# Optimization experiments

Measured on AMD Instinct MI355X. Metric: run time of the kernel, lower is better.

Reference implementation:

```python
import jax, jax.numpy as jnp
import numpy as np

POOL = (7, 7)


def crop_and_resize(image, boxes, box_idx, crop_size):
    """Faithful jnp port of tf.image.crop_and_resize (bilinear, extrapolation_value=0).

    image: [B, H, W, C]; boxes: [N, 4] normalized (y1, x1, y2, x2); box_idx: [N] int.
    Returns [N, ph, pw, C].
    """
    H, W = image.shape[1], image.shape[2]
    ph, pw = crop_size
    y1, x1, y2, x2 = boxes[:, 0], boxes[:, 1], boxes[:, 2], boxes[:, 3]
    iy = jnp.arange(ph, dtype=image.dtype)
    ix = jnp.arange(pw, dtype=image.dtype)
    # sample coords in source-pixel space, TF convention for crop_size > 1
    ys = y1[:, None] * (H - 1) + iy[None, :] * ((y2 - y1)[:, None] * (H - 1) / (ph - 1))  # [N, ph]
    xs = x1[:, None] * (W - 1) + ix[None, :] * ((x2 - x1)[:, None] * (W - 1) / (pw - 1))  # [N, pw]
    vy = (ys >= 0) & (ys <= H - 1)
    vx = (xs >= 0) & (xs <= W - 1)
    y0 = jnp.floor(ys)
    x0 = jnp.floor(xs)
    wy = (ys - y0)[:, :, None, None]   # [N, ph, 1, 1]
    wx = (xs - x0)[:, None, :, None]   # [N, 1, pw, 1]
    y0i = jnp.clip(y0, 0, H - 1).astype(jnp.int32)
    y1i = jnp.clip(y0 + 1, 0, H - 1).astype(jnp.int32)  # when ys is integral, wy==0 so clamp is harmless
    x0i = jnp.clip(x0, 0, W - 1).astype(jnp.int32)
    x1i = jnp.clip(x0 + 1, 0, W - 1).astype(jnp.int32)
    b = box_idx[:, None, None]

    def g(yi, xi):
        return image[b, yi[:, :, None], xi[:, None, :], :]  # [N, ph, pw, C]

    top = g(y0i, x0i) * (1 - wx) + g(y0i, x1i) * wx
    bot = g(y1i, x0i) * (1 - wx) + g(y1i, x1i) * wx
    out = top * (1 - wy) + bot * wy
    valid = (vy[:, :, None] & vx[:, None, :])[..., None]
    return jnp.where(valid, out, jnp.zeros((), image.dtype))


def setup_inputs() -> dict:
    key = jax.random.key(0)
    kb, kp, k3, k4, k5 = jax.random.split(key, 5)
    B, N, C = 2, 1000, 256
    # valid normalized boxes: per-axis sorted uniforms -> y1 <= y2, x1 <= x2
    raw = jax.random.uniform(kb, (B, N, 2, 2), dtype=jnp.float32)  # [..., (y|x), (lo,hi)]
    raw = jnp.sort(raw, axis=-1)
    boxes = jnp.stack([raw[..., 0, 0], raw[..., 1, 0], raw[..., 0, 1], raw[..., 1, 1]], axis=-1)
    return {
        "boxes": boxes,
        "positive_indices": jax.random.randint(kp, (B, N), 0, 2, dtype=jnp.int32),
        "p3": jax.random.normal(k3, (B, 128, 128, C), dtype=jnp.float32),
        "p4": jax.random.normal(k4, (B, 64, 64, C), dtype=jnp.float32),
        "p5": jax.random.normal(k5, (B, 32, 32, C), dtype=jnp.float32),
        "config": 0,
    }


def reference(boxes, positive_indices, p3, p4, p5, config):
    B, N = boxes.shape[0], boxes.shape[1]
    ph, pw = POOL
    h = boxes[..., 2] - boxes[..., 0]
    w = boxes[..., 3] - boxes[..., 1]
    # roi_level = clip(ceil(5 + log2(h*w)), 3, 5); clip in float first (log2(0) -> -inf)
    lvl = jnp.ceil(5.0 + jnp.log(h * w) / jnp.log(2.0))
    roi_level = jnp.clip(lvl, 3.0, 5.0).astype(jnp.int32)  # [B, N]
    boxes_flat = jax.lax.stop_gradient(boxes.reshape(B * N, 4))  # boxes get no grad in original
    lvl_flat = roi_level.reshape(B * N)
    box_idx = jnp.repeat(jnp.arange(B, dtype=jnp.int32), N)
    C = p3.shape[-1]
    pooled = jnp.zeros((B * N, ph, pw, C), dtype=p3.dtype)
    for level, feat in zip((3, 4, 5), (p3, p4, p5)):
        crop = crop_and_resize(feat, boxes_flat, box_idx, POOL)
        mask = (lvl_flat == level)[:, None, None, None]
        pooled = jnp.where(mask, crop, pooled)
    return pooled.reshape(B, N, ph, pw, C)
```

## Files before the change

kernel.cpp:

```cpp
#include <hip/hip_runtime.h>
#include <math.h>


#define N_PER_B 1000
#define NBOX    2000
#define CCH     256
#define PH      7
#define PW      7

__global__ __launch_bounds__(448, 4) void pyramid_roi_align_kernel(
    const float* __restrict__ boxes,
    const float* __restrict__ p3,
    const float* __restrict__ p4,
    const float* __restrict__ p5,
    float* __restrict__ out)
{
    const int box  = blockIdx.x;
    const int iy   = threadIdx.x >> 6;
    const int lane = threadIdx.x & 63;
    const int c    = lane * 4;

    const float y1 = boxes[box * 4 + 0];
    const float x1 = boxes[box * 4 + 1];
    const float y2 = boxes[box * 4 + 2];
    const float x2 = boxes[box * 4 + 3];
    const float h  = y2 - y1;
    const float w  = x2 - x1;

    const float lvl  = ceilf(5.0f + logf(h * w) / 0.69314718055994530942f);
    const float lvlc = fminf(fmaxf(lvl, 3.0f), 5.0f);
    const int level  = (int)lvlc;

    const float* feat;
    int H;
    if (level <= 3)      { feat = p3; H = 128; }
    else if (level == 4) { feat = p4; H = 64;  }
    else                 { feat = p5; H = 32;  }
    const int W = H;

    const int b = (box >= N_PER_B) ? 1 : 0;
    feat += (size_t)b * H * W * CCH;

    const float Hm1 = (float)(H - 1);
    const float Wm1 = (float)(W - 1);

    const float ys = y1 * Hm1 + (float)iy * (h * Hm1 / 6.0f);
    const bool  vy = (ys >= 0.0f) && (ys <= Hm1);

    const float y0f = floorf(ys);
    const float wy  = ys - y0f;
    const float omwy = 1.0f - wy;

    const int y0i = (int)fminf(fmaxf(y0f,        0.0f), Hm1);
    const int y1i = (int)fminf(fmaxf(y0f + 1.0f, 0.0f), Hm1);

    const float* row0 = feat + (size_t)y0i * W * CCH + c;
    const float* row1 = feat + (size_t)y1i * W * CCH + c;

    const float xstep = w * Wm1 / 6.0f;
    float* dst_base = out + ((size_t)box * (PH * PW) + (size_t)iy * PW) * CCH + c;

#pragma unroll
    for (int ix = 0; ix < PW; ++ix) {
        const float xs = x1 * Wm1 + (float)ix * xstep;
        const bool  vx = (xs >= 0.0f) && (xs <= Wm1);

        const float x0f = floorf(xs);
        const float wx  = xs - x0f;
        const float omwx = 1.0f - wx;

        const int x0i = (int)fminf(fmaxf(x0f,        0.0f), Wm1);
        const int x1i = (int)fminf(fmaxf(x0f + 1.0f, 0.0f), Wm1);

        const float4 v00 = *(const float4*)(row0 + (size_t)x0i * CCH);
        const float4 v01 = *(const float4*)(row0 + (size_t)x1i * CCH);
        const float4 v10 = *(const float4*)(row1 + (size_t)x0i * CCH);
        const float4 v11 = *(const float4*)(row1 + (size_t)x1i * CCH);

        float4 res;
        res.x = (v00.x * omwx + v01.x * wx) * omwy + (v10.x * omwx + v11.x * wx) * wy;
        res.y = (v00.y * omwx + v01.y * wx) * omwy + (v10.y * omwx + v11.y * wx) * wy;
        res.z = (v00.z * omwx + v01.z * wx) * omwy + (v10.z * omwx + v11.z * wx) * wy;
        res.w = (v00.w * omwx + v01.w * wx) * omwy + (v10.w * omwx + v11.w * wx) * wy;

        if (!(vy && vx)) { res.x = 0.0f; res.y = 0.0f; res.z = 0.0f; res.w = 0.0f; }

        *(float4*)(dst_base + (size_t)ix * CCH) = res;
    }
}

extern "C" void kernel_launch(void* const* d_in, const int* in_sizes, int n_in,
                              void* d_out, int out_size, void* d_ws, size_t ws_size,
                              hipStream_t stream) {
    const float* boxes = (const float*)d_in[0];
    const float* p3 = (const float*)d_in[2];
    const float* p4 = (const float*)d_in[3];
    const float* p5 = (const float*)d_in[4];
    float* out = (float*)d_out;

    hipLaunchKernelGGL(pyramid_roi_align_kernel, dim3(NBOX), dim3(448), 0, stream,
                       boxes, p3, p4, p5, out);
}
```

Before: 168.9 us.

## Batch all gathers before compute, nontemporal stores, remap waves to 256-thread blocks

Each wave now handles one (box, row) pair and blocks carry 4 waves instead of 7, which changes the block/grid decomposition. All 28 float4 gathers for a row are issued up front, before any interpolation, to raise memory-level parallelism. Output stores become nontemporal so the large write stream does not evict cached feature data. The batched loads raise register pressure, which may lower occupancy.

```diff
diff --git a/kernel.cpp b/kernel.cpp
--- a/kernel.cpp
+++ b/kernel.cpp
@@ -7,18 +7,24 @@
 #define CCH     256
 #define PH      7
 #define PW      7
+#define WAVES_PER_BLOCK 4
+#define TOTAL_WAVES (NBOX * PH)
 
-__global__ __launch_bounds__(448, 4) void pyramid_roi_align_kernel(
+typedef float nfloat4 __attribute__((ext_vector_type(4)));
+
+__global__ __launch_bounds__(256, 3) void pyramid_roi_align_kernel(
     const float* __restrict__ boxes,
     const float* __restrict__ p3,
     const float* __restrict__ p4,
     const float* __restrict__ p5,
     float* __restrict__ out)
 {
-    const int box  = blockIdx.x;
-    const int iy   = threadIdx.x >> 6;
+    const int wave = blockIdx.x * WAVES_PER_BLOCK + (threadIdx.x >> 6);
     const int lane = threadIdx.x & 63;
     const int c    = lane * 4;
+
+    const int box = wave / PH;
+    const int iy  = wave - box * PH;
 
     const float y1 = boxes[box * 4 + 0];
     const float x1 = boxes[box * 4 + 1];
@@ -47,8 +53,8 @@
     const float ys = y1 * Hm1 + (float)iy * (h * Hm1 / 6.0f);
     const bool  vy = (ys >= 0.0f) && (ys <= Hm1);
 
-    const float y0f = floorf(ys);
-    const float wy  = ys - y0f;
+    const float y0f  = floorf(ys);
+    const float wy   = ys - y0f;
     const float omwy = 1.0f - wy;
 
     const int y0i = (int)fminf(fmaxf(y0f,        0.0f), Hm1);
@@ -58,34 +64,38 @@
     const float* row1 = feat + (size_t)y1i * W * CCH + c;
 
     const float xstep = w * Wm1 / 6.0f;
+
+    nfloat4 v00[PW], v01[PW], v10[PW], v11[PW];
+    float   wxv[PW];
+    bool    vxv[PW];
+
+#pragma unroll
+    for (int ix = 0; ix < PW; ++ix) {
+        const float xs = x1 * Wm1 + (float)ix * xstep;
+        vxv[ix] = (xs >= 0.0f) && (xs <= Wm1);
+        const float x0f = floorf(xs);
+        wxv[ix] = xs - x0f;
+        const int x0i = (int)fminf(fmaxf(x0f,        0.0f), Wm1);
+        const int x1i = (int)fminf(fmaxf(x0f + 1.0f, 0.0f), Wm1);
+        v00[ix] = *(const nfloat4*)(row0 + (size_t)x0i * CCH);
+        v01[ix] = *(const nfloat4*)(row0 + (size_t)x1i * CCH);
+        v10[ix] = *(const nfloat4*)(row1 + (size_t)x0i * CCH);
+        v11[ix] = *(const nfloat4*)(row1 + (size_t)x1i * CCH);
+    }
+
     float* dst_base = out + ((size_t)box * (PH * PW) + (size_t)iy * PW) * CCH + c;
 
 #pragma unroll
     for (int ix = 0; ix < PW; ++ix) {
-        const float xs = x1 * Wm1 + (float)ix * xstep;
-        const bool  vx = (xs >= 0.0f) && (xs <= Wm1);
-
-        const float x0f = floorf(xs);
-        const float wx  = xs - x0f;
+        const float wx   = wxv[ix];
         const float omwx = 1.0f - wx;
 
-        const int x0i = (int)fminf(fmaxf(x0f,        0.0f), Wm1);
-        const int x1i = (int)fminf(fmaxf(x0f + 1.0f, 0.0f), Wm1);
+        nfloat4 res = (v00[ix] * omwx + v01[ix] * wx) * omwy
+                    + (v10[ix] * omwx + v11[ix] * wx) * wy;
 
-        const float4 v00 = *(const float4*)(row0 + (size_t)x0i * CCH);
-        const float4 v01 = *(const float4*)(row0 + (size_t)x1i * CCH);
-        const float4 v10 = *(const float4*)(row1 + (size_t)x0i * CCH);
-        const float4 v11 = *(const float4*)(row1 + (size_t)x1i * CCH);
+        if (!(vy && vxv[ix])) res = (nfloat4)0.0f;
 
-        float4 res;
-        res.x = (v00.x * omwx + v01.x * wx) * omwy + (v10.x * omwx + v11.x * wx) * wy;
-        res.y = (v00.y * omwx + v01.y * wx) * omwy + (v10.y * omwx + v11.y * wx) * wy;
-        res.z = (v00.z * omwx + v01.z * wx) * omwy + (v10.z * omwx + v11.z * wx) * wy;
-        res.w = (v00.w * omwx + v01.w * wx) * omwy + (v10.w * omwx + v11.w * wx) * wy;
-
-        if (!(vy && vx)) { res.x = 0.0f; res.y = 0.0f; res.z = 0.0f; res.w = 0.0f; }
-
-        *(float4*)(dst_base + (size_t)ix * CCH) = res;
+        __builtin_nontemporal_store(res, (nfloat4*)(dst_base + (size_t)ix * CCH));
     }
 }
 
@@ -98,6 +108,7 @@
     const float* p5 = (const float*)d_in[4];
     float* out = (float*)d_out;
 
-    hipLaunchKernelGGL(pyramid_roi_align_kernel, dim3(NBOX), dim3(448), 0, stream,
+    const int grid = TOTAL_WAVES / WAVES_PER_BLOCK;
+    hipLaunchKernelGGL(pyramid_roi_align_kernel, dim3(grid), dim3(256), 0, stream,
                        boxes, p3, p4, p5, out);
 }
```

Measured after the change: 169.6 us. About the same (+0.4%).
